# Optimization experiments

Measured on AMD Instinct MI355X. Metric: run time of the kernel, lower is better.

The kernel has to match this reference:

```python
import jax, jax.numpy as jnp
import numpy as np

V, H, B, NS, SL, QL, AL = 100000, 256, 64, 40, 30, 20, 12
NUM_EPISODE = 3


def setup_inputs() -> dict:
    key = jax.random.key(0)
    ks = iter(jax.random.split(key, 48))
    def p(shape, scale=0.05):
        return jax.random.normal(next(ks), shape, jnp.float32) * scale
    d = {}
    d["c_p"] = jax.random.randint(next(ks), (B, NS, SL), 0, V, dtype=jnp.int32)
    d["c_mask"] = jnp.zeros((B, NS, SL), jnp.int32)
    d["q_p"] = jax.random.randint(next(ks), (B, QL), 0, V, dtype=jnp.int32)
    d["q_mask"] = jnp.zeros((B, QL), jnp.int32)
    d["a_I_p"] = jax.random.randint(next(ks), (B, AL), 0, V, dtype=jnp.int32)
    d["a_I_mask"] = jnp.zeros((B, AL), jnp.int32)
    d["a_II_p"] = jax.random.randint(next(ks), (B, AL), 0, V, dtype=jnp.int32)
    d["a_II_mask"] = jnp.zeros((B, AL), jnp.int32)
    d["embed"] = p((V, H)).at[0].set(0.0)  # padding_idx=0
    for name in ["ctx", "q", "ans", "attn", "mem"]:
        d[name + "_Wih"] = p((3 * H, H))
        d[name + "_Whh"] = p((3 * H, H))
        d[name + "_bih"] = p((3 * H,))
        d[name + "_bhh"] = p((3 * H,))
    d["gate_W1"] = p((H, 7 * H)); d["gate_b1"] = p((H,))
    d["gate_W2"] = p((1, H));     d["gate_b2"] = p((1,))
    d["out_W1"] = p((H, 3 * H)); d["out_b1"] = p((H,))
    d["out_W2"] = p((2, H));     d["out_b2"] = p((2,))
    return d


def _gru_step(h, gi_t, Whh, bhh):
    # PyTorch GRU cell math; gates ordered (r, z, n)
    gh = h @ Whh.T + bhh
    i_r, i_z, i_n = jnp.split(gi_t, 3, -1)
    h_r, h_z, h_n = jnp.split(gh, 3, -1)
    r = jax.nn.sigmoid(i_r + h_r)
    z = jax.nn.sigmoid(i_z + h_z)
    n = jnp.tanh(i_n + r * h_n)
    return (1.0 - z) * n + z * h


def _run_gru(x, Wih, Whh, bih, bhh):
    # x: [N, T, H] -> outputs [N, T, H], zero initial hidden
    gi = jnp.einsum('nth,gh->ntg', x, Wih) + bih  # precompute input projections
    h0 = jnp.zeros((x.shape[0], Whh.shape[1]), x.dtype)
    def step(h, g_t):
        h2 = _gru_step(h, g_t, Whh, bhh)
        return h2, h2
    _, outs = jax.lax.scan(step, h0, jnp.swapaxes(gi, 0, 1))
    return jnp.swapaxes(outs, 0, 1)


def _gather_last(outs, mask):
    # real_length = number of zeros in mask (0 marks a valid token)
    lengths = jnp.sum(mask == 0, axis=-1)
    idx = jnp.clip(lengths - 1, 0, outs.shape[1] - 1)
    return jnp.take_along_axis(outs, idx[:, None, None], axis=1)[:, 0]


def _forward(c_p, c_mask, q_p, q_mask, a_I_p, a_I_mask, a_II_p, a_II_mask,
             embed,
             ctx_Wih, ctx_Whh, ctx_bih, ctx_bhh,
             q_Wih, q_Whh, q_bih, q_bhh,
             ans_Wih, ans_Whh, ans_bih, ans_bhh,
             attn_Wih, attn_Whh, attn_bih, attn_bhh,
             mem_Wih, mem_Whh, mem_bih, mem_bhh,
             gate_W1, gate_b1, gate_W2, gate_b2,
             out_W1, out_b1, out_W2, out_b2):
    b, ns, sl = c_p.shape
    # Context encoding: all (batch, sentence) pairs through one batched GRU
    ce = embed[c_p.reshape(b * ns, sl)]                      # [B*NS, SL, H]
    c_out = _run_gru(ce, ctx_Wih, ctx_Whh, ctx_bih, ctx_bhh)
    enc_ctx = _gather_last(c_out, c_mask.reshape(b * ns, sl)).reshape(b, ns, -1)  # [B, NS, H]
    # Question / answers
    enc_q = _gather_last(_run_gru(embed[q_p], q_Wih, q_Whh, q_bih, q_bhh), q_mask)          # [B, H]
    enc_a1 = _gather_last(_run_gru(embed[a_I_p], ans_Wih, ans_Whh, ans_bih, ans_bhh), a_I_mask)
    enc_a2 = _gather_last(_run_gru(embed[a_II_p], ans_Wih, ans_Whh, ans_bih, ans_bhh), a_II_mask)
    # Episodic memory: gated attention GRU scan over context sentences
    ctx_t = jnp.swapaxes(enc_ctx, 0, 1)  # [NS, B, H]
    memory = enc_q
    for _ in range(NUM_EPISODE):
        mem_now = memory
        def step(h, ct):
            feat = jnp.concatenate([ct, mem_now, enc_q, ct * enc_q, ct * mem_now,
                                    jnp.abs(ct - enc_q), jnp.abs(ct - mem_now)], axis=1)  # [B, 7H]
            g = jax.nn.sigmoid(jnp.tanh(feat @ gate_W1.T + gate_b1) @ gate_W2.T + gate_b2)  # [B, 1]
            hc = _gru_step(h, ct @ attn_Wih.T + attn_bih, attn_Whh, attn_bhh)
            return g * hc + (1.0 - g) * h, None
        e, _ = jax.lax.scan(step, jnp.zeros_like(memory), ctx_t)
        memory = _gru_step(memory, e @ mem_Wih.T + mem_bih, mem_Whh, mem_bhh)
    final = jnp.concatenate([memory, enc_a1, enc_a2], axis=1)  # [B, 3H]
    logits = jnp.tanh(final @ out_W1.T + out_b1) @ out_W2.T + out_b2  # [B, 2]
    return jax.nn.softmax(logits, axis=-1)


def reference(c_p, c_mask, q_p, q_mask, a_I_p, a_I_mask, a_II_p, a_II_mask,
              embed,
              ctx_Wih, ctx_Whh, ctx_bih, ctx_bhh,
              q_Wih, q_Whh, q_bih, q_bhh,
              ans_Wih, ans_Whh, ans_bih, ans_bhh,
              attn_Wih, attn_Whh, attn_bih, attn_bhh,
              mem_Wih, mem_Whh, mem_bih, mem_bhh,
              gate_W1, gate_b1, gate_W2, gate_b2,
              out_W1, out_b1, out_W2, out_b2):
    return _forward(c_p, c_mask, q_p, q_mask, a_I_p, a_I_mask, a_II_p, a_II_mask,
                    embed,
                    ctx_Wih, ctx_Whh, ctx_bih, ctx_bhh,
                    q_Wih, q_Whh, q_bih, q_bhh,
                    ans_Wih, ans_Whh, ans_bih, ans_bhh,
                    attn_Wih, attn_Whh, attn_bih, attn_bhh,
                    mem_Wih, mem_Whh, mem_bih, mem_bhh,
                    gate_W1, gate_b1, gate_W2, gate_b2,
                    out_W1, out_b1, out_W2, out_b2)
```

## Files before the change

kernel.cpp:

```cpp
#include <hip/hip_runtime.h>

typedef unsigned short u16;
typedef __bf16 bf16x8 __attribute__((ext_vector_type(8)));
typedef float f32x4 __attribute__((ext_vector_type(4)));

#define NSENT 40
#define SLEN 30
#define QLEN 20
#define ALEN 12
#define SCTX 2560
#define SLOT 24
#define TP 12288

__device__ __forceinline__ float b2f(u16 u){ union{float f; unsigned i;} v; v.i = ((unsigned)u)<<16; return v.f; }
__device__ __forceinline__ u16 f2b(float f){ union{float f; unsigned u;} v; v.f=f; unsigned u=v.u; u += ((u>>16)&1u) + 0x7fffu; return (u16)(u>>16); }
__device__ __forceinline__ float sigm(float x){ return __builtin_amdgcn_rcpf(1.f + __expf(-x)); }
__device__ __forceinline__ float tanh_(float x){
  float a = fminf(fmaxf(2.f*x, -30.f), 30.f);
  float e = __expf(a);
  return 1.f - 2.f*__builtin_amdgcn_rcpf(e + 1.f);
}
__device__ __forceinline__ f32x4 mfma16(bf16x8 a, bf16x8 b, f32x4 c){
  return __builtin_amdgcn_mfma_f32_16x16x32_bf16(a, b, c, 0, 0, 0);
}

__global__ void k_prep(
    const float* cWih, const float* cWhh, const float* qWih, const float* qWhh,
    const float* aWih, const float* aWhh, const float* tWih, const float* tWhh,
    const float* mWih, const float* mWhh, const float* gW1,
    const float* cbih, const float* cbhh, const float* qbih, const float* qbhh,
    const float* abih, const float* abhh, const float* tbih, const float* tbhh,
    const float* mbih, const float* mbhh,
    u16* P0,u16* P1,u16* P2,u16* P3,u16* P4,u16* P5,u16* P6,u16* P7,u16* P8,u16* P9,
    u16* PgW1,
    float* B0,float* B1,float* B2,float* B3,float* B4,float* B5,float* B6,float* B7,
    float* B8,float* B9)
{
  int i = blockIdx.x*512 + threadIdx.x;
  if (i < 1966080){
    int seg = i/196608; int e = i - seg*196608;
    int np = e>>8, k = e&255;
    int g16 = np/48, rem = np - g16*48, gate = rem>>4, cc = rem&15;
    int j = gate*256 + g16*16 + cc;
    const float* S; u16* D;
    switch(seg){
      case 0: S=cWih; D=P0; break; case 1: S=cWhh; D=P1; break;
      case 2: S=qWih; D=P2; break; case 3: S=qWhh; D=P3; break;
      case 4: S=aWih; D=P4; break; case 5: S=aWhh; D=P5; break;
      case 6: S=tWih; D=P6; break; case 7: S=tWhh; D=P7; break;
      case 8: S=mWih; D=P8; break; default: S=mWhh; D=P9; break;
    }
    D[e] = f2b(S[j*256 + k]);
  } else if (i < 2424832){
    int e = i - 1966080;
    PgW1[e] = f2b(gW1[e]);
  } else {
    int e = i - 2424832;
    int seg = e/768; int np = e - seg*768;
    int g16 = np/48, rem = np - g16*48, gate = rem>>4, cc = rem&15;
    int j = gate*256 + g16*16 + cc;
    const float* S; float* D;
    switch(seg){
      case 0: S=cbih; D=B0; break; case 1: S=cbhh; D=B1; break;
      case 2: S=qbih; D=B2; break; case 3: S=qbhh; D=B3; break;
      case 4: S=abih; D=B4; break; case 5: S=abhh; D=B5; break;
      case 6: S=tbih; D=B6; break; case 7: S=tbhh; D=B7; break;
      case 8: S=mbih; D=B8; break; default: S=mbhh; D=B9; break;
    }
    D[np] = S[j];
  }
}

__global__ __launch_bounds__(512, 2) void k_xproj(
    const int* c_p, const int* q_p, const int* a1p, const int* a2p,
    const float* embed,
    const u16* cWihP, const u16* qWihP, const u16* aWihP,
    const float* cBih, const float* qBih, const float* aBih,
    u16* gi_c, u16* gi_q, u16* gi_a1, u16* gi_a2)
{
  __shared__ u16 xb[32][264];
  int bid=blockIdx.x, tid=threadIdx.x;
  const int* toks; const u16* W; const float* bias; u16* out; int T, block, t0;
  if (bid < 2400){ toks=c_p; W=cWihP; bias=cBih; out=gi_c; T=SLEN; block=bid/15; t0=(bid-block*15)*2; }
  else if (bid < 2440){ int e=bid-2400; toks=q_p; W=qWihP; bias=qBih; out=gi_q; T=QLEN; block=e/10; t0=(e-block*10)*2; }
  else if (bid < 2464){ int e=bid-2440; toks=a1p; W=aWihP; bias=aBih; out=gi_a1; T=ALEN; block=e/6; t0=(e-block*6)*2; }
  else               { int e=bid-2464; toks=a2p; W=aWihP; bias=aBih; out=gi_a2; T=ALEN; block=e/6; t0=(e-block*6)*2; }
  int seq0 = block*16;
  #pragma unroll
  for (int p=0;p<4;p++){
    int i=p*512+tid; int row=i>>6, f4=i&63;
    int tp=row>>4, m=row&15;
    int tok = toks[(seq0+m)*T + t0+tp];
    float4 v = *((const float4*)(embed + (long)tok*256) + f4);
    u16* dst = &xb[row][f4*4];
    dst[0]=f2b(v.x); dst[1]=f2b(v.y); dst[2]=f2b(v.z); dst[3]=f2b(v.w);
  }
  const int w=tid>>6, lane=tid&63, c=lane&15, quad=lane>>4;
  f32x4 acc[2][6];
  #pragma unroll
  for (int Mt=0;Mt<2;Mt++)
    #pragma unroll
    for (int nt=0;nt<6;nt++) acc[Mt][nt]=(f32x4){0.f,0.f,0.f,0.f};
  __syncthreads();
  #pragma unroll
  for (int Kt=0;Kt<8;Kt++){
    bf16x8 a0 = *(const bf16x8*)&xb[c][Kt*32+quad*8];
    bf16x8 a1 = *(const bf16x8*)&xb[16+c][Kt*32+quad*8];
    #pragma unroll
    for (int nt=0;nt<6;nt++){
      bf16x8 bfr = *(const bf16x8*)(W + (w*96+nt*16+c)*256 + Kt*32 + quad*8);
      acc[0][nt]=mfma16(a0,bfr,acc[0][nt]);
      acc[1][nt]=mfma16(a1,bfr,acc[1][nt]);
    }
  }
  float biasv[6];
  #pragma unroll
  for (int nt=0;nt<6;nt++) biasv[nt]=bias[w*96+nt*16+c];
  #pragma unroll
  for (int tp=0;tp<2;tp++){
    unsigned d[12];
    #pragma unroll
    for (int k=0;k<12;k++){
      int i0=2*k, i1=2*k+1;
      int r0=i0/6, re0=i0%6, jj0=re0/3, g0=re0%3;
      int r1=i1/6, re1=i1%6, jj1=re1/3, g1=re1%3;
      unsigned lo=f2b(acc[tp][jj0*3+g0][r0]+biasv[jj0*3+g0]);
      unsigned hi=f2b(acc[tp][jj1*3+g1][r1]+biasv[jj1*3+g1]);
      d[k] = lo | (hi<<16);
    }
    u16* dst = out + ((long)(block*T + t0+tp))*TP + (w*64+lane)*SLOT;
    *(uint4*)(dst)    = *(uint4*)&d[0];
    *(uint4*)(dst+8)  = *(uint4*)&d[4];
    *(uint4*)(dst+16) = *(uint4*)&d[8];
  }
}

__global__ __launch_bounds__(512, 2) void k_enc_scan(
    const int* c_mask, const int* q_mask, const int* a1m, const int* a2m,
    const u16* cWhhP, const u16* qWhhP, const u16* aWhhP,
    const float* cBhh, const float* qBhh, const float* aBhh,
    const u16* gi_c, const u16* gi_q, const u16* gi_a1, const u16* gi_a2,
    u16* enc_hi, u16* enc_lo, float* enc_qf, float* enc_a1f, float* enc_a2f)
{
  __shared__ u16 hhi[16][264];
  __shared__ u16 hlo[16][264];
  __shared__ int idxs[16];
  int bid=blockIdx.x, tid=threadIdx.x;
  const int* msk; const u16* W; const float* bhh; const u16* gi; int T, seq0, mode;
  u16 *ohi=0, *olo=0; float* of=0;
  if (bid<160){ msk=c_mask; W=cWhhP; bhh=cBhh; gi=gi_c+(long)bid*SLEN*TP; T=SLEN; seq0=bid*16; mode=0; ohi=enc_hi; olo=enc_lo; }
  else if (bid<164){ int e=bid-160; msk=q_mask; W=qWhhP; bhh=qBhh; gi=gi_q+(long)e*QLEN*TP; T=QLEN; seq0=e*16; mode=1; of=enc_qf; }
  else if (bid<168){ int e=bid-164; msk=a1m; W=aWhhP; bhh=aBhh; gi=gi_a1+(long)e*ALEN*TP; T=ALEN; seq0=e*16; mode=1; of=enc_a1f; }
  else             { int e=bid-168; msk=a2m; W=aWhhP; bhh=aBhh; gi=gi_a2+(long)e*ALEN*TP; T=ALEN; seq0=e*16; mode=1; of=enc_a2f; }
  if (tid<16){
    int len=0; const int* mr=msk+(seq0+tid)*T;
    for (int t=0;t<T;t++) len += (mr[t]==0);
    int id=len-1; if(id<0)id=0; if(id>T-1)id=T-1; idxs[tid]=id;
  }
  for (int i=tid;i<16*264;i+=512){ ((u16*)hhi)[i]=0; ((u16*)hlo)[i]=0; }
  const int w=tid>>6, lane=tid&63, c=lane&15, quad=lane>>4;
  float biasv[6];
  #pragma unroll
  for (int nt=0;nt<6;nt++) biasv[nt]=bhh[w*96+nt*16+c];
  uint4 breg[48];
  #pragma unroll
  for (int nt=0;nt<6;nt++)
    #pragma unroll
    for (int Kt=0;Kt<8;Kt++)
      breg[nt*8+Kt] = *(const uint4*)(W + (w*96+nt*16+c)*256 + Kt*32 + quad*8);
  float hreg[8];
  #pragma unroll
  for (int i=0;i<8;i++) hreg[i]=0.f;
  const u16* gp = gi + (w*64+lane)*SLOT;
  uint4 pA0=*(const uint4*)(gp), pA1=*(const uint4*)(gp+8), pA2=*(const uint4*)(gp+16);
  __syncthreads();
  int idxr[4];
  #pragma unroll
  for (int r=0;r<4;r++) idxr[r]=idxs[quad*4+r];

  for (int t=0;t<T;t++){
    uint4 pB0,pB1,pB2;
    bool pf=(t+1<T);
    if (pf){
      const u16* gn = gp + (long)(t+1)*TP;
      pB0=*(const uint4*)(gn); pB1=*(const uint4*)(gn+8); pB2=*(const uint4*)(gn+16);
    }
    f32x4 acc[6];
    #pragma unroll
    for (int nt=0;nt<6;nt++) acc[nt]=(f32x4){0.f,0.f,0.f,0.f};
    #pragma unroll
    for (int Kt=0;Kt<8;Kt++){
      bf16x8 a=*(const bf16x8*)&hhi[c][Kt*32+quad*8];
      #pragma unroll
      for (int nt=0;nt<6;nt++) acc[nt]=mfma16(a,*(const bf16x8*)&breg[nt*8+Kt],acc[nt]);
    }
    #pragma unroll
    for (int Kt=0;Kt<8;Kt++){
      bf16x8 a=*(const bf16x8*)&hlo[c][Kt*32+quad*8];
      #pragma unroll
      for (int nt=0;nt<6;nt++) acc[nt]=mfma16(a,*(const bf16x8*)&breg[nt*8+Kt],acc[nt]);
    }
    unsigned pd[12];
    *(uint4*)&pd[0]=pA0; *(uint4*)&pd[4]=pA1; *(uint4*)&pd[8]=pA2;
    #pragma unroll
    for (int r=0;r<4;r++){
      int m=quad*4+r;
      #pragma unroll
      for (int jj=0;jj<2;jj++){
        int j=w*32+jj*16+c;
        int ib=(r*2+jj)*3;
        float ir = b2f((u16)((pd[ib>>1]     >> ((ib&1)*16)) & 0xffffu));
        float iz = b2f((u16)((pd[(ib+1)>>1] >> (((ib+1)&1)*16)) & 0xffffu));
        float in_= b2f((u16)((pd[(ib+2)>>1] >> (((ib+2)&1)*16)) & 0xffffu));
        float hr=acc[jj*3+0][r]+biasv[jj*3+0];
        float hz=acc[jj*3+1][r]+biasv[jj*3+1];
        float hn=acc[jj*3+2][r]+biasv[jj*3+2];
        float rr=sigm(ir+hr), zz=sigm(iz+hz), nn=tanh_(in_+rr*hn);
        float ho=hreg[r*2+jj];
        float hnew=(1.f-zz)*nn+zz*ho;
        hreg[r*2+jj]=hnew;
        u16 hi_=f2b(hnew); u16 lo_=f2b(hnew-b2f(hi_));
        hhi[m][j]=hi_; hlo[m][j]=lo_;
        if (t==idxr[r]){
          long o=(long)(seq0+m)*256+j;
          if (mode==0){ ohi[o]=hi_; olo[o]=lo_; }
          else of[o]=hnew;
        }
      }
    }
    __syncthreads();
    pA0=pB0; pA1=pB1; pA2=pB2;
  }
}

__global__ __launch_bounds__(512, 2) void k_gi(
    const u16* enc_hi, const u16* enc_lo, const u16* tWihP, const float* tBih,
    float* gi_attn, const float* enc_qf, float* mem_f)
{
  int bid=blockIdx.x, tid=threadIdx.x;
  if (bid==160){ for (int i=tid;i<64*256;i+=512) mem_f[i]=enc_qf[i]; return; }
  __shared__ u16 ahi[16][264];
  __shared__ u16 alo[16][264];
  int bblk=bid/40, s=bid-bblk*40, b0=bblk*16;
  {
    int row=tid>>5, ch=tid&31;
    long seq=(long)(b0+row)*NSENT + s;
    *(uint4*)((char*)&ahi[row][0]+ch*16) = *((const uint4*)(enc_hi+seq*256)+ch);
    *(uint4*)((char*)&alo[row][0]+ch*16) = *((const uint4*)(enc_lo+seq*256)+ch);
  }
  const int w=tid>>6, lane=tid&63, c=lane&15, quad=lane>>4;
  f32x4 acc[6];
  #pragma unroll
  for (int nt=0;nt<6;nt++) acc[nt]=(f32x4){0.f,0.f,0.f,0.f};
  __syncthreads();
  #pragma unroll
  for (int Kt=0;Kt<8;Kt++){
    bf16x8 a=*(const bf16x8*)&ahi[c][Kt*32+quad*8];
    #pragma unroll
    for (int nt=0;nt<6;nt++){
      bf16x8 bfr=*(const bf16x8*)(tWihP + (w*96+nt*16+c)*256 + Kt*32 + quad*8);
      acc[nt]=mfma16(a,bfr,acc[nt]);
    }
  }
  #pragma unroll
  for (int Kt=0;Kt<8;Kt++){
    bf16x8 a=*(const bf16x8*)&alo[c][Kt*32+quad*8];
    #pragma unroll
    for (int nt=0;nt<6;nt++){
      bf16x8 bfr=*(const bf16x8*)(tWihP + (w*96+nt*16+c)*256 + Kt*32 + quad*8);
      acc[nt]=mfma16(a,bfr,acc[nt]);
    }
  }
  float biasv[6];
  #pragma unroll
  for (int nt=0;nt<6;nt++) biasv[nt]=tBih[w*96+nt*16+c];
  float* dst = gi_attn + ((long)(bblk*40+s))*TP + (w*64+lane)*SLOT;
  #pragma unroll
  for (int d=0;d<6;d++){
    float4 v;
    #pragma unroll
    for (int e=0;e<4;e++){
      int idx=4*d+e;
      int r=idx/6, rem=idx%6, jj=rem/3, g=rem%3;
      ((float*)&v)[e]=acc[jj*3+g][r]+biasv[jj*3+g];
    }
    *(float4*)(dst+4*d)=v;
  }
}

__global__ __launch_bounds__(512, 1) void k_gatepre(
    const u16* enc_hi, const u16* enc_lo, const float* enc_qf,
    const u16* W1, const float* b1, float* partial)
{
  __shared__ float ctf[32][257];
  __shared__ float qvf[32][257];
  __shared__ u16 ab[32][264];
  int bid=blockIdx.x, tid=threadIdx.x, seq0=bid*32;
  #pragma unroll
  for (int p=0;p<16;p++){
    int i=p*512+tid; int row=i>>8, j=i&255;
    int grow=seq0+row; int b=grow/NSENT;
    ctf[row][j]=b2f(enc_hi[(long)grow*256+j])+b2f(enc_lo[(long)grow*256+j]);
    qvf[row][j]=enc_qf[b*256+j];
  }
  const int w=tid>>6, lane=tid&63, c=lane&15, quad=lane>>4;
  f32x4 acc[2][2];
  #pragma unroll
  for (int nt=0;nt<2;nt++){
    float bv=b1[(w*2+nt)*16+c];
    acc[0][nt]=(f32x4){bv,bv,bv,bv}; acc[1][nt]=acc[0][nt];
  }
  const int chl[4]={0,2,3,5};
  for (int ci=0; ci<4; ci++){
    int ch=chl[ci];
    __syncthreads();
    #pragma unroll
    for (int p=0;p<16;p++){
      int i=p*512+tid; int row=i>>8, j=i&255;
      float ct=ctf[row][j], qv=qvf[row][j];
      float v;
      if      (ch==0) v=ct;
      else if (ch==2) v=qv;
      else if (ch==3) v=ct*qv;
      else            v=fabsf(ct-qv);
      ab[row][j]=f2b(v);
    }
    __syncthreads();
    #pragma unroll
    for (int Kt=0;Kt<8;Kt++){
      bf16x8 a0=*(const bf16x8*)&ab[c][Kt*32+quad*8];
      bf16x8 a1=*(const bf16x8*)&ab[16+c][Kt*32+quad*8];
      #pragma unroll
      for (int nt=0;nt<2;nt++){
        int n=(w*2+nt)*16+c;
        bf16x8 bfr=*(const bf16x8*)(W1 + (long)n*1792 + ch*256 + Kt*32 + quad*8);
        acc[0][nt]=mfma16(a0,bfr,acc[0][nt]);
        acc[1][nt]=mfma16(a1,bfr,acc[1][nt]);
      }
    }
  }
  #pragma unroll
  for (int Mt=0;Mt<2;Mt++)
    #pragma unroll
    for (int nt=0;nt<2;nt++)
      #pragma unroll
      for (int r=0;r<4;r++)
        partial[(long)(seq0+Mt*16+quad*4+r)*256 + (w*2+nt)*16+c] = acc[Mt][nt][r];
}

__global__ __launch_bounds__(512, 1) void k_gate(
    const u16* enc_hi, const u16* enc_lo, const float* mem_f,
    const float* partial, const u16* W1, const float* W2, const float* b2v, float* g)
{
  __shared__ float ctf[32][257];
  __shared__ float mvf[32][257];
  __shared__ u16 ab[32][264];
  __shared__ float pl[32][8];
  int bid=blockIdx.x, tid=threadIdx.x, seq0=bid*32;
  #pragma unroll
  for (int p=0;p<16;p++){
    int i=p*512+tid; int row=i>>8, j=i&255;
    int grow=seq0+row; int b=grow/NSENT;
    ctf[row][j]=b2f(enc_hi[(long)grow*256+j])+b2f(enc_lo[(long)grow*256+j]);
    mvf[row][j]=mem_f[b*256+j];
  }
  const int w=tid>>6, lane=tid&63, c=lane&15, quad=lane>>4;
  f32x4 acc[2][2];
  float w2v[2];
  #pragma unroll
  for (int nt=0;nt<2;nt++){
    int n=(w*2+nt)*16+c;
    w2v[nt]=W2[n];
    #pragma unroll
    for (int Mt=0;Mt<2;Mt++)
      #pragma unroll
      for (int r=0;r<4;r++)
        acc[Mt][nt][r]=partial[(long)(seq0+Mt*16+quad*4+r)*256 + n];
  }
  const int chl[3]={1,4,6};
  for (int ci=0; ci<3; ci++){
    int ch=chl[ci];
    __syncthreads();
    #pragma unroll
    for (int p=0;p<16;p++){
      int i=p*512+tid; int row=i>>8, j=i&255;
      float ct=ctf[row][j], mv=mvf[row][j];
      float v;
      if      (ch==1) v=mv;
      else if (ch==4) v=ct*mv;
      else            v=fabsf(ct-mv);
      ab[row][j]=f2b(v);
    }
    __syncthreads();
    #pragma unroll
    for (int Kt=0;Kt<8;Kt++){
      bf16x8 a0=*(const bf16x8*)&ab[c][Kt*32+quad*8];
      bf16x8 a1=*(const bf16x8*)&ab[16+c][Kt*32+quad*8];
      #pragma unroll
      for (int nt=0;nt<2;nt++){
        int n=(w*2+nt)*16+c;
        bf16x8 bfr=*(const bf16x8*)(W1 + (long)n*1792 + ch*256 + Kt*32 + quad*8);
        acc[0][nt]=mfma16(a0,bfr,acc[0][nt]);
        acc[1][nt]=mfma16(a1,bfr,acc[1][nt]);
      }
    }
  }
  float pm[8];
  #pragma unroll
  for (int i=0;i<8;i++){
    int Mt=i>>2, r=i&3;
    float s=0.f;
    #pragma unroll
    for (int nt=0;nt<2;nt++) s += tanh_(acc[Mt][nt][r])*w2v[nt];
    pm[i]=s;
  }
  #pragma unroll
  for (int off=1;off<16;off<<=1)
    #pragma unroll
    for (int i=0;i<8;i++) pm[i]+=__shfl_xor(pm[i],off,64);
  if (c==0){
    #pragma unroll
    for (int i=0;i<8;i++){ int m=(i>>2)*16+quad*4+(i&3); pl[m][w]=pm[i]; }
  }
  __syncthreads();
  if (tid<32){
    float s=b2v[0];
    #pragma unroll
    for (int ww=0;ww<8;ww++) s+=pl[tid][ww];
    g[seq0+tid]=sigm(s);
  }
}

__global__ __launch_bounds__(512, 2) void k_scan(
    const u16* tWhhP, const float* tBhh,
    const float* gi_attn, const float* g,
    float* mem_f, const u16* mWihP, const u16* mWhhP,
    const float* mBih, const float* mBhh)
{
  __shared__ u16 hb[16][264];
  __shared__ u16 mhi[16][264];
  __shared__ u16 mlo[16][264];
  __shared__ float memfl[16][256];
  __shared__ float gl[16][40];
  int bid=blockIdx.x, tid=threadIdx.x, b0=bid*16;
  const int w=tid>>6, lane=tid&63, c=lane&15, quad=lane>>4;
  for (int i=tid;i<16*264;i+=512){ ((u16*)hb)[i]=0; }
  for (int i=tid;i<4096;i+=512){
    int m=i>>8, j=i&255;
    float v=mem_f[(b0+m)*256+j]; memfl[m][j]=v;
    u16 hi_=f2b(v); mhi[m][j]=hi_; mlo[m][j]=f2b(v-b2f(hi_));
  }
  for (int i=tid;i<640;i+=512){ int m=i/40, s=i-m*40; gl[m][s]=g[(b0+m)*40+s]; }
  float biasv[6];
  #pragma unroll
  for (int nt=0;nt<6;nt++) biasv[nt]=tBhh[w*96+nt*16+c];
  uint4 breg[48];
  #pragma unroll
  for (int nt=0;nt<6;nt++)
    #pragma unroll
    for (int Kt=0;Kt<8;Kt++)
      breg[nt*8+Kt] = *(const uint4*)(tWhhP + (w*96+nt*16+c)*256 + Kt*32 + quad*8);
  float hreg[8];
  #pragma unroll
  for (int i=0;i<8;i++) hreg[i]=0.f;
  const float* gp = gi_attn + ((long)bid*NSENT)*TP + (w*64+lane)*SLOT;
  float4 pA[6];
  #pragma unroll
  for (int d=0;d<6;d++) pA[d]=*(const float4*)(gp+4*d);
  __syncthreads();

  for (int s=0;s<NSENT;s++){
    float4 pB[6];
    bool pf=(s+1<NSENT);
    if (pf){
      const float* gn = gp + (long)(s+1)*TP;
      #pragma unroll
      for (int d=0;d<6;d++) pB[d]=*(const float4*)(gn+4*d);
    }
    f32x4 acc[6];
    #pragma unroll
    for (int nt=0;nt<6;nt++) acc[nt]=(f32x4){0.f,0.f,0.f,0.f};
    #pragma unroll
    for (int Kt=0;Kt<8;Kt++){
      bf16x8 a=*(const bf16x8*)&hb[c][Kt*32+quad*8];
      #pragma unroll
      for (int nt=0;nt<6;nt++) acc[nt]=mfma16(a,*(const bf16x8*)&breg[nt*8+Kt],acc[nt]);
    }
    const float* pf32 = (const float*)&pA[0];
    #pragma unroll
    for (int r=0;r<4;r++){
      int m=quad*4+r;
      float gv = gl[m][s];
      #pragma unroll
      for (int jj=0;jj<2;jj++){
        int j=w*32+jj*16+c;
        int ib=(r*2+jj)*3;
        float ir=pf32[ib], iz=pf32[ib+1], in_=pf32[ib+2];
        float hr=acc[jj*3+0][r]+biasv[jj*3+0];
        float hz=acc[jj*3+1][r]+biasv[jj*3+1];
        float hn=acc[jj*3+2][r]+biasv[jj*3+2];
        float rr=sigm(ir+hr), zz=sigm(iz+hz), nn=tanh_(in_+rr*hn);
        float ho=hreg[r*2+jj];
        float hc=(1.f-zz)*nn+zz*ho;
        float hnew=gv*hc+(1.f-gv)*ho;
        hreg[r*2+jj]=hnew;
        hb[m][j]=f2b(hnew);
      }
    }
    __syncthreads();
    #pragma unroll
    for (int d=0;d<6;d++) pA[d]=pB[d];
  }
  f32x4 ai[6], ah[6];
  #pragma unroll
  for (int nt=0;nt<6;nt++){ ai[nt]=(f32x4){0.f,0.f,0.f,0.f}; ah[nt]=ai[nt]; }
  #pragma unroll
  for (int Kt=0;Kt<8;Kt++){
    bf16x8 a=*(const bf16x8*)&hb[c][Kt*32+quad*8];
    #pragma unroll
    for (int nt=0;nt<6;nt++){
      bf16x8 bfr=*(const bf16x8*)(mWihP + (w*96+nt*16+c)*256 + Kt*32 + quad*8);
      ai[nt]=mfma16(a,bfr,ai[nt]);
    }
  }
  #pragma unroll
  for (int Kt=0;Kt<8;Kt++){
    bf16x8 a=*(const bf16x8*)&mhi[c][Kt*32+quad*8];
    #pragma unroll
    for (int nt=0;nt<6;nt++){
      bf16x8 bfr=*(const bf16x8*)(mWhhP + (w*96+nt*16+c)*256 + Kt*32 + quad*8);
      ah[nt]=mfma16(a,bfr,ah[nt]);
    }
  }
  #pragma unroll
  for (int Kt=0;Kt<8;Kt++){
    bf16x8 a=*(const bf16x8*)&mlo[c][Kt*32+quad*8];
    #pragma unroll
    for (int nt=0;nt<6;nt++){
      bf16x8 bfr=*(const bf16x8*)(mWhhP + (w*96+nt*16+c)*256 + Kt*32 + quad*8);
      ah[nt]=mfma16(a,bfr,ah[nt]);
    }
  }
  float bih6[6], bhh6[6];
  #pragma unroll
  for (int nt=0;nt<6;nt++){ bih6[nt]=mBih[w*96+nt*16+c]; bhh6[nt]=mBhh[w*96+nt*16+c]; }
  #pragma unroll
  for (int r=0;r<4;r++){
    int m=quad*4+r;
    #pragma unroll
    for (int jj=0;jj<2;jj++){
      int j=w*32+jj*16+c;
      float ir=ai[jj*3+0][r]+bih6[jj*3+0];
      float iz=ai[jj*3+1][r]+bih6[jj*3+1];
      float in_=ai[jj*3+2][r]+bih6[jj*3+2];
      float hr=ah[jj*3+0][r]+bhh6[jj*3+0];
      float hz=ah[jj*3+1][r]+bhh6[jj*3+1];
      float hn=ah[jj*3+2][r]+bhh6[jj*3+2];
      float rr=sigm(ir+hr), zz=sigm(iz+hz), nn=tanh_(in_+rr*hn);
      float mo=memfl[m][j];
      mem_f[(b0+m)*256+j]=(1.f-zz)*nn+zz*mo;
    }
  }
}

__global__ void k_final(const float* mem_f, const float* a1f, const float* a2f,
    const float* W1o, const float* b1o, const float* W2o, const float* b2o, float* outp)
{
  __shared__ float af[768];
  __shared__ float tl[256];
  __shared__ float lg[2];
  int b=blockIdx.x, tid=threadIdx.x;
  af[tid]     = mem_f[b*256+tid];
  af[256+tid] = a1f[b*256+tid];
  af[512+tid] = a2f[b*256+tid];
  __syncthreads();
  float s=b1o[tid];
  const float* wr=W1o + (long)tid*768;
  for (int k=0;k<768;k++) s += af[k]*wr[k];
  tl[tid]=tanh_(s);
  __syncthreads();
  if (tid<2){
    float l=b2o[tid];
    const float* w2=W2o + tid*256;
    for (int k=0;k<256;k++) l += tl[k]*w2[k];
    lg[tid]=l;
  }
  __syncthreads();
  if (tid==0){
    float m=fmaxf(lg[0],lg[1]);
    float e0=__expf(lg[0]-m), e1=__expf(lg[1]-m);
    float inv=1.f/(e0+e1);
    outp[b*2]=e0*inv; outp[b*2+1]=e1*inv;
  }
}

extern "C" void kernel_launch(void* const* d_in, const int* in_sizes, int n_in,
                              void* d_out, int out_size, void* d_ws, size_t ws_size,
                              hipStream_t stream) {
  const int* c_p   = (const int*)d_in[0];
  const int* c_m   = (const int*)d_in[1];
  const int* q_p   = (const int*)d_in[2];
  const int* q_m   = (const int*)d_in[3];
  const int* a1p   = (const int*)d_in[4];
  const int* a1m   = (const int*)d_in[5];
  const int* a2p   = (const int*)d_in[6];
  const int* a2m   = (const int*)d_in[7];
  const float* embed = (const float*)d_in[8];
  const float* cWih=(const float*)d_in[9],  *cWhh=(const float*)d_in[10], *cbih=(const float*)d_in[11], *cbhh=(const float*)d_in[12];
  const float* qWih=(const float*)d_in[13], *qWhh=(const float*)d_in[14], *qbih=(const float*)d_in[15], *qbhh=(const float*)d_in[16];
  const float* aWih=(const float*)d_in[17], *aWhh=(const float*)d_in[18], *abih=(const float*)d_in[19], *abhh=(const float*)d_in[20];
  const float* tWih=(const float*)d_in[21], *tWhh=(const float*)d_in[22], *tbih=(const float*)d_in[23], *tbhh=(const float*)d_in[24];
  const float* mWih=(const float*)d_in[25], *mWhh=(const float*)d_in[26], *mbih=(const float*)d_in[27], *mbhh=(const float*)d_in[28];
  const float* gW1=(const float*)d_in[29], *gb1=(const float*)d_in[30], *gW2=(const float*)d_in[31], *gb2=(const float*)d_in[32];
  const float* oW1=(const float*)d_in[33], *ob1=(const float*)d_in[34], *oW2=(const float*)d_in[35], *ob2=(const float*)d_in[36];

  char* ws = (char*)d_ws;
  size_t off = 0;
  u16* P[10];
  for (int i=0;i<10;i++){ P[i]=(u16*)(ws+off); off+=393216; }
  u16* PgW1 =(u16*)(ws+off); off+=917504;
  float* B[10];
  for (int i=0;i<10;i++){ B[i]=(float*)(ws+off); off+=3072; }
  u16* gi_c =(u16*)(ws+off); off+=(size_t)160*SLEN*TP*2;
  u16* gi_q =(u16*)(ws+off); off+=(size_t)4*QLEN*TP*2;
  u16* gi_a1=(u16*)(ws+off); off+=(size_t)4*ALEN*TP*2;
  u16* gi_a2=(u16*)(ws+off); off+=(size_t)4*ALEN*TP*2;
  u16* enc_hi=(u16*)(ws+off); off+=(size_t)SCTX*256*2;
  u16* enc_lo=(u16*)(ws+off); off+=(size_t)SCTX*256*2;
  float* enc_qf =(float*)(ws+off); off+=64*256*4;
  float* enc_a1f=(float*)(ws+off); off+=64*256*4;
  float* enc_a2f=(float*)(ws+off); off+=64*256*4;
  float* mem_f  =(float*)(ws+off); off+=64*256*4;
  float* gi_attn=(float*)(ws+off); off+=(size_t)160*TP*4;
  float* partial=(float*)(ws+off); off+=(size_t)SCTX*256*4;
  float* gbuf   =(float*)(ws+off); off+=SCTX*4;

  k_prep<<<4751, 512, 0, stream>>>(cWih,cWhh,qWih,qWhh,aWih,aWhh,tWih,tWhh,mWih,mWhh,gW1,
      cbih,cbhh,qbih,qbhh,abih,abhh,tbih,tbhh,mbih,mbhh,
      P[0],P[1],P[2],P[3],P[4],P[5],P[6],P[7],P[8],P[9], PgW1,
      B[0],B[1],B[2],B[3],B[4],B[5],B[6],B[7],B[8],B[9]);

  k_xproj<<<2488, 512, 0, stream>>>(c_p,q_p,a1p,a2p, embed,
      P[0],P[2],P[4], B[0],B[2],B[4], gi_c,gi_q,gi_a1,gi_a2);

  k_enc_scan<<<172, 512, 0, stream>>>(c_m,q_m,a1m,a2m,
      P[1],P[3],P[5], B[1],B[3],B[5], gi_c,gi_q,gi_a1,gi_a2,
      enc_hi,enc_lo, enc_qf,enc_a1f,enc_a2f);

  k_gi<<<161, 512, 0, stream>>>(enc_hi,enc_lo, P[6], B[6], gi_attn, enc_qf, mem_f);

  k_gatepre<<<80, 512, 0, stream>>>(enc_hi,enc_lo, enc_qf, PgW1, gb1, partial);

  for (int ep=0; ep<3; ep++){
    k_gate<<<80, 512, 0, stream>>>(enc_hi,enc_lo, mem_f, partial, PgW1, gW2, gb2, gbuf);
    k_scan<<<4, 512, 0, stream>>>(P[7], B[7], gi_attn, gbuf, mem_f, P[8], P[9], B[8], B[9]);
  }

  k_final<<<64, 256, 0, stream>>>(mem_f, enc_a1f, enc_a2f, oW1, ob1, oW2, ob2, (float*)d_out);
}
```

Before: 936.5 us.

## Double xproj tile to 32 sequences and split gate-input layout into halves

The input-projection kernel now handles 32 sequences per block instead of 16, so each weight fragment loaded from global memory feeds four MFMA row tiles instead of two. The grid is halved and occupancy hints are raised. Embedding loads and gate-input stores use nontemporal hints. The per-timestep gate-input layout is split into two 12-element halves (one per jj group), and the scan kernel reads it with six 8-byte loads in place of three 16-byte loads. The intent is to cut redundant weight traffic and register pressure in xproj, at the cost of more, smaller loads in the scan.

```diff
diff --git a/kernel.cpp b/kernel.cpp
--- a/kernel.cpp
+++ b/kernel.cpp
@@ -3,6 +3,8 @@
 typedef unsigned short u16;
 typedef __bf16 bf16x8 __attribute__((ext_vector_type(8)));
 typedef float f32x4 __attribute__((ext_vector_type(4)));
+typedef float f32x4v __attribute__((ext_vector_type(4)));
+typedef unsigned int u32x2 __attribute__((ext_vector_type(2)));
 
 #define NSENT 40
 #define SLEN 30
@@ -71,67 +73,80 @@
   }
 }
 
-__global__ __launch_bounds__(512, 2) void k_xproj(
+__global__ __launch_bounds__(512, 4) void k_xproj(
     const int* c_p, const int* q_p, const int* a1p, const int* a2p,
     const float* embed,
     const u16* cWihP, const u16* qWihP, const u16* aWihP,
     const float* cBih, const float* qBih, const float* aBih,
     u16* gi_c, u16* gi_q, u16* gi_a1, u16* gi_a2)
 {
-  __shared__ u16 xb[32][264];
+  __shared__ u16 xb[64][288];
   int bid=blockIdx.x, tid=threadIdx.x;
-  const int* toks; const u16* W; const float* bias; u16* out; int T, block, t0;
-  if (bid < 2400){ toks=c_p; W=cWihP; bias=cBih; out=gi_c; T=SLEN; block=bid/15; t0=(bid-block*15)*2; }
-  else if (bid < 2440){ int e=bid-2400; toks=q_p; W=qWihP; bias=qBih; out=gi_q; T=QLEN; block=e/10; t0=(e-block*10)*2; }
-  else if (bid < 2464){ int e=bid-2440; toks=a1p; W=aWihP; bias=aBih; out=gi_a1; T=ALEN; block=e/6; t0=(e-block*6)*2; }
-  else               { int e=bid-2464; toks=a2p; W=aWihP; bias=aBih; out=gi_a2; T=ALEN; block=e/6; t0=(e-block*6)*2; }
-  int seq0 = block*16;
-  #pragma unroll
-  for (int p=0;p<4;p++){
+  const int* toks; const u16* W; const float* bias; u16* out; int T, blk32, t0;
+  if (bid < 1200){ toks=c_p; W=cWihP; bias=cBih; out=gi_c; T=SLEN; blk32=bid/15; t0=(bid-blk32*15)*2; }
+  else if (bid < 1220){ int e=bid-1200; toks=q_p; W=qWihP; bias=qBih; out=gi_q; T=QLEN; blk32=e/10; t0=(e-blk32*10)*2; }
+  else if (bid < 1232){ int e=bid-1220; toks=a1p; W=aWihP; bias=aBih; out=gi_a1; T=ALEN; blk32=e/6; t0=(e-blk32*6)*2; }
+  else               { int e=bid-1232; toks=a2p; W=aWihP; bias=aBih; out=gi_a2; T=ALEN; blk32=e/6; t0=(e-blk32*6)*2; }
+  int seq0 = blk32*32;
+  #pragma unroll
+  for (int p=0;p<8;p++){
     int i=p*512+tid; int row=i>>6, f4=i&63;
-    int tp=row>>4, m=row&15;
-    int tok = toks[(seq0+m)*T + t0+tp];
-    float4 v = *((const float4*)(embed + (long)tok*256) + f4);
-    u16* dst = &xb[row][f4*4];
-    dst[0]=f2b(v.x); dst[1]=f2b(v.y); dst[2]=f2b(v.z); dst[3]=f2b(v.w);
+    int tp=row>>5, sm=row&31;
+    int tok = toks[(seq0+sm)*T + t0+tp];
+    f32x4v v = __builtin_nontemporal_load((const f32x4v*)(embed + (long)tok*256) + f4);
+    unsigned lo = (unsigned)f2b(v[0]) | ((unsigned)f2b(v[1])<<16);
+    unsigned hi = (unsigned)f2b(v[2]) | ((unsigned)f2b(v[3])<<16);
+    u32x2 pk; pk.x=lo; pk.y=hi;
+    *(u32x2*)&xb[row][f4*4] = pk;
   }
   const int w=tid>>6, lane=tid&63, c=lane&15, quad=lane>>4;
-  f32x4 acc[2][6];
-  #pragma unroll
-  for (int Mt=0;Mt<2;Mt++)
-    #pragma unroll
-    for (int nt=0;nt<6;nt++) acc[Mt][nt]=(f32x4){0.f,0.f,0.f,0.f};
-  __syncthreads();
-  #pragma unroll
-  for (int Kt=0;Kt<8;Kt++){
-    bf16x8 a0 = *(const bf16x8*)&xb[c][Kt*32+quad*8];
-    bf16x8 a1 = *(const bf16x8*)&xb[16+c][Kt*32+quad*8];
-    #pragma unroll
-    for (int nt=0;nt<6;nt++){
-      bf16x8 bfr = *(const bf16x8*)(W + (w*96+nt*16+c)*256 + Kt*32 + quad*8);
-      acc[0][nt]=mfma16(a0,bfr,acc[0][nt]);
-      acc[1][nt]=mfma16(a1,bfr,acc[1][nt]);
-    }
-  }
-  float biasv[6];
-  #pragma unroll
-  for (int nt=0;nt<6;nt++) biasv[nt]=bias[w*96+nt*16+c];
-  #pragma unroll
-  for (int tp=0;tp<2;tp++){
-    unsigned d[12];
-    #pragma unroll
-    for (int k=0;k<12;k++){
-      int i0=2*k, i1=2*k+1;
-      int r0=i0/6, re0=i0%6, jj0=re0/3, g0=re0%3;
-      int r1=i1/6, re1=i1%6, jj1=re1/3, g1=re1%3;
-      unsigned lo=f2b(acc[tp][jj0*3+g0][r0]+biasv[jj0*3+g0]);
-      unsigned hi=f2b(acc[tp][jj1*3+g1][r1]+biasv[jj1*3+g1]);
-      d[k] = lo | (hi<<16);
-    }
-    u16* dst = out + ((long)(block*T + t0+tp))*TP + (w*64+lane)*SLOT;
-    *(uint4*)(dst)    = *(uint4*)&d[0];
-    *(uint4*)(dst+8)  = *(uint4*)&d[4];
-    *(uint4*)(dst+16) = *(uint4*)&d[8];
+  __syncthreads();
+  #pragma unroll
+  for (int jj=0;jj<2;jj++){
+    f32x4 acc[4][3];
+    #pragma unroll
+    for (int Mt=0;Mt<4;Mt++)
+      #pragma unroll
+      for (int g=0;g<3;g++) acc[Mt][g]=(f32x4){0.f,0.f,0.f,0.f};
+    #pragma unroll
+    for (int Kt=0;Kt<8;Kt++){
+      bf16x8 a0=*(const bf16x8*)&xb[c][Kt*32+quad*8];
+      bf16x8 a1=*(const bf16x8*)&xb[16+c][Kt*32+quad*8];
+      bf16x8 a2=*(const bf16x8*)&xb[32+c][Kt*32+quad*8];
+      bf16x8 a3=*(const bf16x8*)&xb[48+c][Kt*32+quad*8];
+      #pragma unroll
+      for (int g=0;g<3;g++){
+        bf16x8 bfr=*(const bf16x8*)(W + (w*96+(jj*3+g)*16+c)*256 + Kt*32 + quad*8);
+        acc[0][g]=mfma16(a0,bfr,acc[0][g]);
+        acc[1][g]=mfma16(a1,bfr,acc[1][g]);
+        acc[2][g]=mfma16(a2,bfr,acc[2][g]);
+        acc[3][g]=mfma16(a3,bfr,acc[3][g]);
+      }
+    }
+    float bv[3];
+    #pragma unroll
+    for (int g=0;g<3;g++) bv[g]=bias[w*96+(jj*3+g)*16+c];
+    #pragma unroll
+    for (int Mt=0;Mt<4;Mt++){
+      int tp=Mt>>1, smh=Mt&1;
+      unsigned d[6];
+      #pragma unroll
+      for (int k=0;k<6;k++){
+        int s0=2*k, s1=2*k+1;
+        int r0=s0/3, g0=s0%3, r1=s1/3, g1=s1%3;
+        unsigned lo=f2b(acc[Mt][g0][r0]+bv[g0]);
+        unsigned hi=f2b(acc[Mt][g1][r1]+bv[g1]);
+        d[k]=lo|(hi<<16);
+      }
+      long block16 = (long)blk32*2 + smh;
+      u16* dst = out + (block16*T + t0+tp)*TP + jj*6144 + (w*64+lane)*12;
+      u32x2 s0v; s0v.x=d[0]; s0v.y=d[1];
+      u32x2 s1v; s1v.x=d[2]; s1v.y=d[3];
+      u32x2 s2v; s2v.x=d[4]; s2v.y=d[5];
+      __builtin_nontemporal_store(s0v, (u32x2*)dst);
+      __builtin_nontemporal_store(s1v, (u32x2*)(dst+4));
+      __builtin_nontemporal_store(s2v, (u32x2*)(dst+8));
+    }
   }
 }
 
@@ -171,19 +186,21 @@
   float hreg[8];
   #pragma unroll
   for (int i=0;i<8;i++) hreg[i]=0.f;
-  const u16* gp = gi + (w*64+lane)*SLOT;
-  uint4 pA0=*(const uint4*)(gp), pA1=*(const uint4*)(gp+8), pA2=*(const uint4*)(gp+16);
+  const u16* gp = gi + (w*64+lane)*12;
+  u32x2 pA0=*(const u32x2*)(gp),      pA1=*(const u32x2*)(gp+4),    pA2=*(const u32x2*)(gp+8);
+  u32x2 pA3=*(const u32x2*)(gp+6144), pA4=*(const u32x2*)(gp+6148), pA5=*(const u32x2*)(gp+6152);
   __syncthreads();
   int idxr[4];
   #pragma unroll
   for (int r=0;r<4;r++) idxr[r]=idxs[quad*4+r];
 
   for (int t=0;t<T;t++){
-    uint4 pB0,pB1,pB2;
+    u32x2 pB0,pB1,pB2,pB3,pB4,pB5;
     bool pf=(t+1<T);
     if (pf){
       const u16* gn = gp + (long)(t+1)*TP;
-      pB0=*(const uint4*)(gn); pB1=*(const uint4*)(gn+8); pB2=*(const uint4*)(gn+16);
+      pB0=*(const u32x2*)(gn);      pB1=*(const u32x2*)(gn+4);    pB2=*(const u32x2*)(gn+8);
+      pB3=*(const u32x2*)(gn+6144); pB4=*(const u32x2*)(gn+6148); pB5=*(const u32x2*)(gn+6152);
     }
     f32x4 acc[6];
     #pragma unroll
@@ -201,17 +218,18 @@
       for (int nt=0;nt<6;nt++) acc[nt]=mfma16(a,*(const bf16x8*)&breg[nt*8+Kt],acc[nt]);
     }
     unsigned pd[12];
-    *(uint4*)&pd[0]=pA0; *(uint4*)&pd[4]=pA1; *(uint4*)&pd[8]=pA2;
+    *(u32x2*)&pd[0]=pA0; *(u32x2*)&pd[2]=pA1; *(u32x2*)&pd[4]=pA2;
+    *(u32x2*)&pd[6]=pA3; *(u32x2*)&pd[8]=pA4; *(u32x2*)&pd[10]=pA5;
     #pragma unroll
     for (int r=0;r<4;r++){
       int m=quad*4+r;
       #pragma unroll
       for (int jj=0;jj<2;jj++){
         int j=w*32+jj*16+c;
-        int ib=(r*2+jj)*3;
-        float ir = b2f((u16)((pd[ib>>1]     >> ((ib&1)*16)) & 0xffffu));
-        float iz = b2f((u16)((pd[(ib+1)>>1] >> (((ib+1)&1)*16)) & 0xffffu));
-        float in_= b2f((u16)((pd[(ib+2)>>1] >> (((ib+2)&1)*16)) & 0xffffu));
+        int ib=r*3;
+        float ir = b2f((u16)((pd[jj*6+(ib>>1)]     >> ((ib&1)*16)) & 0xffffu));
+        float iz = b2f((u16)((pd[jj*6+((ib+1)>>1)] >> (((ib+1)&1)*16)) & 0xffffu));
+        float in_= b2f((u16)((pd[jj*6+((ib+2)>>1)] >> (((ib+2)&1)*16)) & 0xffffu));
         float hr=acc[jj*3+0][r]+biasv[jj*3+0];
         float hz=acc[jj*3+1][r]+biasv[jj*3+1];
         float hn=acc[jj*3+2][r]+biasv[jj*3+2];
@@ -229,7 +247,7 @@
       }
     }
     __syncthreads();
-    pA0=pB0; pA1=pB1; pA2=pB2;
+    pA0=pB0; pA1=pB1; pA2=pB2; pA3=pB3; pA4=pB4; pA5=pB5;
   }
 }
 
@@ -640,7 +658,7 @@
       P[0],P[1],P[2],P[3],P[4],P[5],P[6],P[7],P[8],P[9], PgW1,
       B[0],B[1],B[2],B[3],B[4],B[5],B[6],B[7],B[8],B[9]);
 
-  k_xproj<<<2488, 512, 0, stream>>>(c_p,q_p,a1p,a2p, embed,
+  k_xproj<<<1244, 512, 0, stream>>>(c_p,q_p,a1p,a2p, embed,
       P[0],P[2],P[4], B[0],B[2],B[4], gi_c,gi_q,gi_a1,gi_a2);
 
   k_enc_scan<<<172, 512, 0, stream>>>(c_m,q_m,a1m,a2m,
```

Result: faster. 893.6 us (median of 2 runs) (-4.6%).
